# Optimization experiments

Hardware: AMD Instinct MI355X
Metric: run time of the kernel (lower is better)

The kernel has to match this reference:

```python
import jax, jax.numpy as jnp
import numpy as np

B, H, I, E = 16, 16, 512, 512  # batch, heads, input_dim, embedding_dim (I must == E for matmul(q,k))


def setup_inputs() -> dict:
    key = jax.random.key(0)
    k_x, k_q, k_k, k_v, k_w, k_b = jax.random.split(key, 6)
    return {
        "x": jax.random.normal(k_x, (B, 1, I, E), dtype=jnp.float32),
        "W_q": jax.random.normal(k_q, (1, H, I, E), dtype=jnp.float32),
        "W_k": jax.random.normal(k_k, (1, H, I, E), dtype=jnp.float32),
        "W_v": jax.random.normal(k_v, (1, H, I, E), dtype=jnp.float32),
        "mlp_w": jax.random.normal(k_w, (E, E), dtype=jnp.float32) * (1.0 / np.sqrt(E)),
        "mlp_b": jnp.zeros((E,), dtype=jnp.float32),
    }


def reference(x, W_q, W_k, W_v, mlp_w, mlp_b):
    # Broadcast elementwise "projections": [B,1,I,E] * [1,H,I,E] -> [B,H,I,E]
    q = x * W_q
    k = x * W_k
    v = x * W_v
    scale = jnp.sqrt(jnp.asarray(E, dtype=x.dtype))
    # matmul with NO transpose of keys (as in the original): [B,H,I,E]@[B,H,I,E] needs E==I
    scores = jnp.matmul(q, k) / scale            # [B,H,I,I]
    attn = jax.nn.softmax(scores, axis=2)        # softmax over dim=2 (rows), faithful to source
    emb = jnp.sum(jnp.matmul(attn, v), axis=2)   # [B,H,I,E] summed over I -> [B,H,E]
    return emb @ mlp_w.T + mlp_b                 # nn.Linear: x @ W^T + b -> [B,H,E]
```

## Files before the change

### kernel.cpp

```cpp
#include <hip/hip_runtime.h>
#include <hip/hip_bf16.h>

#define B_ 16
#define H_ 16
#define I_ 512
#define E_ 512


#define NSLICE 16
#define KSPLIT 8

__global__ __launch_bounds__(256) void k_emb_part(const float* __restrict__ x,
                                                  const float* __restrict__ Wv,
                                                  float* __restrict__ part) {
    const int e     = blockIdx.x * 64 + (threadIdx.x & 63);
    const int b0    = blockIdx.y * 8;
    const int h0    = (blockIdx.z & 1) * 8;
    const int slice = blockIdx.z >> 1;
    const int lane  = threadIdx.x & 63;
    const int wave  = threadIdx.x >> 6;

    float acc[8][8];
#pragma unroll
    for (int bi = 0; bi < 8; ++bi)
#pragma unroll
        for (int hj = 0; hj < 8; ++hj) acc[bi][hj] = 0.0f;

    const int ibase = slice * 32 + wave * 8;
    const float* xp[8];
    const float* wp[8];
#pragma unroll
    for (int bi = 0; bi < 8; ++bi)
        xp[bi] = x + ((size_t)(b0 + bi) * I_ + ibase) * E_ + e;
#pragma unroll
    for (int hj = 0; hj < 8; ++hj)
        wp[hj] = Wv + ((size_t)(h0 + hj) * I_ + ibase) * E_ + e;

    for (int ii = 0; ii < 8; ++ii) {
        const int off = ii * E_;
        float xv[8], wv[8];
#pragma unroll
        for (int bi = 0; bi < 8; ++bi) xv[bi] = xp[bi][off];
#pragma unroll
        for (int hj = 0; hj < 8; ++hj) wv[hj] = wp[hj][off];
#pragma unroll
        for (int bi = 0; bi < 8; ++bi)
#pragma unroll
            for (int hj = 0; hj < 8; ++hj)
                acc[bi][hj] = fmaf(xv[bi], wv[hj], acc[bi][hj]);
    }

    __shared__ float red[4][64][64];
#pragma unroll
    for (int bi = 0; bi < 8; ++bi)
#pragma unroll
        for (int hj = 0; hj < 8; ++hj)
            red[wave][bi * 8 + hj][lane] = acc[bi][hj];
    __syncthreads();

    for (int t = threadIdx.x; t < 64 * 64; t += 256) {
        const int pair = t >> 6, le = t & 63;
        float s = (red[0][pair][le] + red[1][pair][le]) +
                  (red[2][pair][le] + red[3][pair][le]);
        const int row = (b0 + (pair >> 3)) * H_ + h0 + (pair & 7);
        part[((size_t)slice * (B_ * H_) + row) * E_ + blockIdx.x * 64 + le] = s;
    }
}

__global__ __launch_bounds__(256) void k_emb_reduce(const float4* __restrict__ part,
                                                    float4* __restrict__ emb) {
    const int idx = blockIdx.x * 256 + threadIdx.x;
    const int sl  = (B_ * H_ * E_) / 4;
    float4 s = part[idx];
#pragma unroll
    for (int j = 1; j < NSLICE; ++j) {
        float4 p = part[(size_t)j * sl + idx];
        s.x += p.x; s.y += p.y; s.z += p.z; s.w += p.w;
    }
    emb[idx] = s;
}

__global__ __launch_bounds__(128) void k_mlp_part(const float* __restrict__ emb,
                                                  const float* __restrict__ W,
                                                  float* __restrict__ part) {
    const int cblk = blockIdx.x;
    const int rblk = blockIdx.y;
    const int k0   = blockIdx.z * 64;

    __shared__ float As[32][68];
    __shared__ float Ws[64][68];

    const int t = threadIdx.x;

    {
        const int r8 = t >> 4, kq = t & 15;
#pragma unroll
        for (int it = 0; it < 4; ++it) {
            const int r = r8 + it * 8;
            float4 v = *(const float4*)(emb + (size_t)(rblk * 32 + r) * E_ + k0 + kq * 4);
            *(float4*)&As[r][kq * 4] = v;
        }
    }
    {
        const int c8 = t >> 4, kq = t & 15;
#pragma unroll
        for (int it = 0; it < 8; ++it) {
            const int c = c8 + it * 8;
            float4 v = *(const float4*)(W + (size_t)(cblk * 64 + c) * E_ + k0 + kq * 4);
            Ws[kq * 4 + 0][c] = v.x;
            Ws[kq * 4 + 1][c] = v.y;
            Ws[kq * 4 + 2][c] = v.z;
            Ws[kq * 4 + 3][c] = v.w;
        }
    }
    __syncthreads();

    const int tx = t & 15, ty = t >> 4;
    const int c0 = tx * 4, r0 = ty * 4;

    float4 acc0 = {0, 0, 0, 0}, acc1 = {0, 0, 0, 0};
    float4 acc2 = {0, 0, 0, 0}, acc3 = {0, 0, 0, 0};

    for (int k = 0; k < 64; k += 4) {
        float4 a0 = *(const float4*)&As[r0 + 0][k];
        float4 a1 = *(const float4*)&As[r0 + 1][k];
        float4 a2 = *(const float4*)&As[r0 + 2][k];
        float4 a3 = *(const float4*)&As[r0 + 3][k];
        float4 w0 = *(const float4*)&Ws[k + 0][c0];
        float4 w1 = *(const float4*)&Ws[k + 1][c0];
        float4 w2 = *(const float4*)&Ws[k + 2][c0];
        float4 w3 = *(const float4*)&Ws[k + 3][c0];
#define MLP_STEP(ACC, AV)                                                  \
        ACC.x = fmaf(AV.x, w0.x, fmaf(AV.y, w1.x, fmaf(AV.z, w2.x, fmaf(AV.w, w3.x, ACC.x)))); \
        ACC.y = fmaf(AV.x, w0.y, fmaf(AV.y, w1.y, fmaf(AV.z, w2.y, fmaf(AV.w, w3.y, ACC.y)))); \
        ACC.z = fmaf(AV.x, w0.z, fmaf(AV.y, w1.z, fmaf(AV.z, w2.z, fmaf(AV.w, w3.z, ACC.z)))); \
        ACC.w = fmaf(AV.x, w0.w, fmaf(AV.y, w1.w, fmaf(AV.z, w2.w, fmaf(AV.w, w3.w, ACC.w))));
        MLP_STEP(acc0, a0)
        MLP_STEP(acc1, a1)
        MLP_STEP(acc2, a2)
        MLP_STEP(acc3, a3)
#undef MLP_STEP
    }

    float* dst = part + ((size_t)blockIdx.z * (B_ * H_) + rblk * 32 + r0) * E_ +
                 cblk * 64 + c0;
    *(float4*)(dst + 0 * E_) = acc0;
    *(float4*)(dst + 1 * E_) = acc1;
    *(float4*)(dst + 2 * E_) = acc2;
    *(float4*)(dst + 3 * E_) = acc3;
}

__global__ __launch_bounds__(256) void k_out(const float4* __restrict__ part,
                                             const float4* __restrict__ bias,
                                             float4* __restrict__ out) {
    const int idx = blockIdx.x * 256 + threadIdx.x;
    const int sl  = (B_ * H_ * E_) / 4;
    float4 s = part[idx];
#pragma unroll
    for (int j = 1; j < KSPLIT; ++j) {
        float4 p = part[(size_t)j * sl + idx];
        s.x += p.x; s.y += p.y; s.z += p.z; s.w += p.w;
    }
    float4 bv = bias[idx & (E_ / 4 - 1)];
    s.x += bv.x; s.y += bv.y; s.z += bv.z; s.w += bv.w;
    out[idx] = s;
}

extern "C" void kernel_launch(void* const* d_in, const int* in_sizes, int n_in,
                              void* d_out, int out_size, void* d_ws, size_t ws_size,
                              hipStream_t stream) {
    const float* x     = (const float*)d_in[0];
    const float* W_v   = (const float*)d_in[3];
    const float* mlp_w = (const float*)d_in[4];
    const float* mlp_b = (const float*)d_in[5];
    float* out = (float*)d_out;

    float* epart = (float*)d_ws;
    float* emb   = epart + (size_t)NSLICE * B_ * H_ * E_;
    float* mpart = emb + (size_t)B_ * H_ * E_;

    dim3 g1(E_ / 64, B_ / 8, (H_ / 8) * NSLICE);
    k_emb_part<<<g1, 256, 0, stream>>>(x, W_v, epart);

    k_emb_reduce<<<(B_ * H_ * E_ / 4) / 256, 256, 0, stream>>>(
        (const float4*)epart, (float4*)emb);

    dim3 g3(E_ / 64, (B_ * H_) / 32, KSPLIT);
    k_mlp_part<<<g3, 128, 0, stream>>>(emb, mlp_w, mpart);

    k_out<<<(B_ * H_ * E_ / 4) / 256, 256, 0, stream>>>(
        (const float4*)mpart, (const float4*)mlp_b, (float4*)out);
}
```

Baseline: 112.7 us.

## Fuse all four stages into one cooperative kernel with grid syncs

Combines the partial embedding, slice reduction, split-K MLP and output reduction into one cooperative-launched kernel separated by grid-wide barriers, with shared memory reused across phases. This removes three kernel launches and their inter-kernel gaps. In exchange, grid syncs add barrier cost and the reduction phases use only a quarter of each block's threads. A fallback to the original four-launch path remains in case the cooperative launch fails.

Measured after the change: 292.0 us. +159.1%, slower.

```diff
diff --git a/kernel.cpp b/kernel.cpp
--- a/kernel.cpp
+++ b/kernel.cpp
@@ -1,5 +1,7 @@
 #include <hip/hip_runtime.h>
-#include <hip/hip_bf16.h>
+#include <hip/hip_cooperative_groups.h>
+
+namespace cg = cooperative_groups;
 
 #define B_ 16
 #define H_ 16
@@ -9,6 +11,160 @@
 
 #define NSLICE 16
 #define KSPLIT 8
+
+#define MLP_STEP(ACC, AV)                                                  \
+    ACC.x = fmaf(AV.x, w0.x, fmaf(AV.y, w1.x, fmaf(AV.z, w2.x, fmaf(AV.w, w3.x, ACC.x)))); \
+    ACC.y = fmaf(AV.x, w0.y, fmaf(AV.y, w1.y, fmaf(AV.z, w2.y, fmaf(AV.w, w3.y, ACC.y)))); \
+    ACC.z = fmaf(AV.x, w0.z, fmaf(AV.y, w1.z, fmaf(AV.z, w2.z, fmaf(AV.w, w3.z, ACC.z)))); \
+    ACC.w = fmaf(AV.x, w0.w, fmaf(AV.y, w1.w, fmaf(AV.z, w2.w, fmaf(AV.w, w3.w, ACC.w))));
+
+__global__ __launch_bounds__(256, 2) void k_fused(
+    const float* __restrict__ x, const float* __restrict__ Wv,
+    const float* __restrict__ W, const float* __restrict__ bias,
+    float* __restrict__ epart, float* __restrict__ emb,
+    float* __restrict__ mpart, float* __restrict__ out) {
+    __shared__ __align__(16) float lds[16384];
+    const int bid = blockIdx.x;
+    const int t   = (int)threadIdx.x;
+
+    {
+        const int ex    = bid & 7;
+        const int by    = (bid >> 3) & 1;
+        const int bz    = bid >> 4;
+        const int e     = ex * 64 + (t & 63);
+        const int b0    = by * 8;
+        const int h0    = (bz & 1) * 8;
+        const int slice = bz >> 1;
+        const int lane  = t & 63;
+        const int wave  = t >> 6;
+
+        float acc[8][8];
+#pragma unroll
+        for (int bi = 0; bi < 8; ++bi)
+#pragma unroll
+            for (int hj = 0; hj < 8; ++hj) acc[bi][hj] = 0.0f;
+
+        const int ibase = slice * 32 + wave * 8;
+        const float* xp[8];
+        const float* wp[8];
+#pragma unroll
+        for (int bi = 0; bi < 8; ++bi)
+            xp[bi] = x + ((size_t)(b0 + bi) * I_ + ibase) * E_ + e;
+#pragma unroll
+        for (int hj = 0; hj < 8; ++hj)
+            wp[hj] = Wv + ((size_t)(h0 + hj) * I_ + ibase) * E_ + e;
+
+        for (int ii = 0; ii < 8; ++ii) {
+            const int off = ii * E_;
+            float xv[8], wv[8];
+#pragma unroll
+            for (int bi = 0; bi < 8; ++bi) xv[bi] = xp[bi][off];
+#pragma unroll
+            for (int hj = 0; hj < 8; ++hj) wv[hj] = wp[hj][off];
+#pragma unroll
+            for (int bi = 0; bi < 8; ++bi)
+#pragma unroll
+                for (int hj = 0; hj < 8; ++hj)
+                    acc[bi][hj] = fmaf(xv[bi], wv[hj], acc[bi][hj]);
+        }
+
+        float (*red)[64][64] = (float (*)[64][64])lds;
+#pragma unroll
+        for (int bi = 0; bi < 8; ++bi)
+#pragma unroll
+            for (int hj = 0; hj < 8; ++hj)
+                red[wave][bi * 8 + hj][lane] = acc[bi][hj];
+        __syncthreads();
+
+        for (int tt = t; tt < 64 * 64; tt += 256) {
+            const int pair = tt >> 6, le = tt & 63;
+            float s = (red[0][pair][le] + red[1][pair][le]) +
+                      (red[2][pair][le] + red[3][pair][le]);
+            const int row = (b0 + (pair >> 3)) * H_ + h0 + (pair & 7);
+            epart[((size_t)slice * (B_ * H_) + row) * E_ + ex * 64 + le] = s;
+        }
+    }
+    cg::this_grid().sync();
+
+    if (t < 64) {
+        const int idx = bid * 64 + t;
+        const int sl  = (B_ * H_ * E_) / 4;
+        const float4* p = (const float4*)epart;
+        float4 s = p[idx];
+#pragma unroll
+        for (int j = 1; j < NSLICE; ++j) {
+            float4 v = p[(size_t)j * sl + idx];
+            s.x += v.x; s.y += v.y; s.z += v.z; s.w += v.w;
+        }
+        ((float4*)emb)[idx] = s;
+    }
+    cg::this_grid().sync();
+
+    {
+        const int cblk = bid & 7;
+        const int rblk = (bid >> 3) & 7;
+        const int kch  = bid >> 6;
+        const int k0   = kch * 64;
+
+        float (*As)[68] = (float (*)[68])lds;
+        float (*Ws)[68] = (float (*)[68])(lds + 32 * 68);
+
+#pragma unroll
+        for (int it = 0; it < 2; ++it) {
+            const int f = t + it * 256;
+            const int r = f >> 4, kq = f & 15;
+            float4 v = *(const float4*)(emb + (size_t)(rblk * 32 + r) * E_ + k0 + kq * 4);
+            *(float4*)&As[r][kq * 4] = v;
+        }
+#pragma unroll
+        for (int it = 0; it < 4; ++it) {
+            const int f = t + it * 256;
+            const int c = f >> 4, kq = f & 15;
+            float4 v = *(const float4*)(W + (size_t)(cblk * 64 + c) * E_ + k0 + kq * 4);
+            Ws[kq * 4 + 0][c] = v.x;
+            Ws[kq * 4 + 1][c] = v.y;
+            Ws[kq * 4 + 2][c] = v.z;
+            Ws[kq * 4 + 3][c] = v.w;
+        }
+        __syncthreads();
+
+        const int tx = t & 15, ty = t >> 4;
+        const int c0 = tx * 4, r0 = ty * 2;
+
+        float4 acc0 = {0, 0, 0, 0}, acc1 = {0, 0, 0, 0};
+        for (int k = 0; k < 64; k += 4) {
+            float4 a0 = *(const float4*)&As[r0 + 0][k];
+            float4 a1 = *(const float4*)&As[r0 + 1][k];
+            float4 w0 = *(const float4*)&Ws[k + 0][c0];
+            float4 w1 = *(const float4*)&Ws[k + 1][c0];
+            float4 w2 = *(const float4*)&Ws[k + 2][c0];
+            float4 w3 = *(const float4*)&Ws[k + 3][c0];
+            MLP_STEP(acc0, a0)
+            MLP_STEP(acc1, a1)
+        }
+
+        float* dst = mpart + ((size_t)kch * (B_ * H_) + rblk * 32 + r0) * E_ +
+                     cblk * 64 + c0;
+        *(float4*)(dst + 0 * E_) = acc0;
+        *(float4*)(dst + 1 * E_) = acc1;
+    }
+    cg::this_grid().sync();
+
+    if (t < 64) {
+        const int idx = bid * 64 + t;
+        const int sl  = (B_ * H_ * E_) / 4;
+        const float4* p = (const float4*)mpart;
+        float4 s = p[idx];
+#pragma unroll
+        for (int j = 1; j < KSPLIT; ++j) {
+            float4 v = p[(size_t)j * sl + idx];
+            s.x += v.x; s.y += v.y; s.z += v.z; s.w += v.w;
+        }
+        float4 bv = ((const float4*)bias)[idx & (E_ / 4 - 1)];
+        s.x += bv.x; s.y += bv.y; s.z += bv.z; s.w += bv.w;
+        ((float4*)out)[idx] = s;
+    }
+}
 
 __global__ __launch_bounds__(256) void k_emb_part(const float* __restrict__ x,
                                                   const float* __restrict__ Wv,
@@ -91,7 +247,6 @@
     __shared__ float Ws[64][68];
 
     const int t = threadIdx.x;
-
     {
         const int r8 = t >> 4, kq = t & 15;
 #pragma unroll
@@ -130,16 +285,10 @@
         float4 w1 = *(const float4*)&Ws[k + 1][c0];
         float4 w2 = *(const float4*)&Ws[k + 2][c0];
         float4 w3 = *(const float4*)&Ws[k + 3][c0];
-#define MLP_STEP(ACC, AV)                                                  \
-        ACC.x = fmaf(AV.x, w0.x, fmaf(AV.y, w1.x, fmaf(AV.z, w2.x, fmaf(AV.w, w3.x, ACC.x)))); \
-        ACC.y = fmaf(AV.x, w0.y, fmaf(AV.y, w1.y, fmaf(AV.z, w2.y, fmaf(AV.w, w3.y, ACC.y)))); \
-        ACC.z = fmaf(AV.x, w0.z, fmaf(AV.y, w1.z, fmaf(AV.z, w2.z, fmaf(AV.w, w3.z, ACC.z)))); \
-        ACC.w = fmaf(AV.x, w0.w, fmaf(AV.y, w1.w, fmaf(AV.z, w2.w, fmaf(AV.w, w3.w, ACC.w))));
         MLP_STEP(acc0, a0)
         MLP_STEP(acc1, a1)
         MLP_STEP(acc2, a2)
         MLP_STEP(acc3, a3)
-#undef MLP_STEP
     }
 
     float* dst = part + ((size_t)blockIdx.z * (B_ * H_) + rblk * 32 + r0) * E_ +
@@ -179,15 +328,19 @@
     float* emb   = epart + (size_t)NSLICE * B_ * H_ * E_;
     float* mpart = emb + (size_t)B_ * H_ * E_;
 
-    dim3 g1(E_ / 64, B_ / 8, (H_ / 8) * NSLICE);
-    k_emb_part<<<g1, 256, 0, stream>>>(x, W_v, epart);
-
-    k_emb_reduce<<<(B_ * H_ * E_ / 4) / 256, 256, 0, stream>>>(
-        (const float4*)epart, (float4*)emb);
-
-    dim3 g3(E_ / 64, (B_ * H_) / 32, KSPLIT);
-    k_mlp_part<<<g3, 128, 0, stream>>>(emb, mlp_w, mpart);
-
-    k_out<<<(B_ * H_ * E_ / 4) / 256, 256, 0, stream>>>(
-        (const float4*)mpart, (const float4*)mlp_b, (float4*)out);
-}
+    void* args[] = {(void*)&x,     (void*)&W_v, (void*)&mlp_w, (void*)&mlp_b,
+                    (void*)&epart, (void*)&emb, (void*)&mpart, (void*)&out};
+    hipError_t err = hipLaunchCooperativeKernel((const void*)k_fused, dim3(512),
+                                                dim3(256), args, 0, stream);
+    if (err != hipSuccess) {
+        (void)hipGetLastError();
+        dim3 g1(E_ / 64, B_ / 8, (H_ / 8) * NSLICE);
+        k_emb_part<<<g1, 256, 0, stream>>>(x, W_v, epart);
+        k_emb_reduce<<<(B_ * H_ * E_ / 4) / 256, 256, 0, stream>>>(
+            (const float4*)epart, (float4*)emb);
+        dim3 g3(E_ / 64, (B_ * H_) / 32, KSPLIT);
+        k_mlp_part<<<g3, 128, 0, stream>>>(emb, mlp_w, mpart);
+        k_out<<<(B_ * H_ * E_ / 4) / 256, 256, 0, stream>>>(
+            (const float4*)mpart, (const float4*)mlp_b, (float4*)out);
+    }
+}
```
